# Kernel optimization log

Measured on AMD Instinct MI355X. Metric: run time of the kernel, lower is better.

Reference implementation:

```python
import jax, jax.numpy as jnp
import numpy as np

N = 100000     # total points
PBS = 500      # point_batch_size (hard-coded in module)
K = 100        # num_neighbors
KP = 15        # num_kernel_points
EPS = 1e-5


def _bn(x, g, b, axes):
    # torch BatchNorm in training mode: batch stats, biased variance
    m = jnp.mean(x, axis=axes, keepdims=True)
    v = jnp.var(x, axis=axes, keepdims=True)
    return (x - m) / jnp.sqrt(v + EPS) * g + b


def setup_inputs() -> dict:
    key = jax.random.key(0)
    ks = jax.random.split(key, 16)
    rn = lambda k, sh, s=1.0: jax.random.normal(k, sh, jnp.float32) * s
    return {
        "pts": rn(ks[0], (N, 3)),
        "normal": rn(ks[1], (N, 3)),
        "kp_points": rn(ks[2], (KP, 3)),
        "kp_weights": rn(ks[3], (KP, 3, 128), 0.3),
        "kp_sigma": jnp.float32(1.0),
        "conv1_w": rn(ks[4], (1024, 128), 128 ** -0.5),
        "conv1_b": rn(ks[5], (1024,), 0.02),
        "bn1_g": jnp.ones((1024,), jnp.float32),
        "bn1_b": jnp.zeros((1024,), jnp.float32),
        "fc1_w": rn(ks[6], (512, 1024), 1024 ** -0.5),
        "fc1_b": rn(ks[7], (512,), 0.02),
        "bn4_g": jnp.ones((512,), jnp.float32),
        "bn4_b": jnp.zeros((512,), jnp.float32),
        "fc2_w": rn(ks[8], (256, 512), 512 ** -0.5),
        "fc2_b": rn(ks[9], (256,), 0.02),
        "bn5_g": jnp.ones((256,), jnp.float32),
        "bn5_b": jnp.zeros((256,), jnp.float32),
        "fc3_w": rn(ks[10], (3, 256), 256 ** -0.5),
        "fc3_b": rn(ks[11], (3,), 0.02),
        "index": jax.random.randint(ks[12], (PBS,), 0, N, jnp.int32),
    }


def reference(pts, normal, kp_points, kp_weights, kp_sigma,
              conv1_w, conv1_b, bn1_g, bn1_b,
              fc1_w, fc1_b, bn4_g, bn4_b,
              fc2_w, fc2_b, bn5_g, bn5_b,
              fc3_w, fc3_b, index):
    sel = pts[index]                                               # [B,3]
    # L-inf pairwise distance and kNN (topk of -dist, as in the torch code)
    dist = jnp.max(jnp.abs(sel[:, None, :] - pts[None, :, :]), axis=-1)  # [B,N]
    _, nbr = jax.lax.top_k(-dist, K)                               # [B,K]
    rel = pts[nbr] - sel[:, None, :]                               # [B,K,3]

    # KPConv: gaussian weights vs kernel points, per-kernel-point linear map
    d2 = jnp.sum((rel[:, :, None, :] - kp_points[None, None]) ** 2, axis=-1)  # [B,K,KP]
    w = jnp.exp(-0.5 * d2 / (kp_sigma ** 2))
    wf = rel[:, :, None, :] * w[..., None]                         # [B,K,KP,3]
    h = jax.nn.relu(jnp.einsum('bnkc,kco->bno', wf, kp_weights))   # [B,K,128]

    # 1x1 conv 128->1024, relu then BN over (batch, points) per channel
    h = jnp.einsum('bnc,oc->bno', h, conv1_w) + conv1_b            # [B,K,1024]
    h = _bn(jax.nn.relu(h), bn1_g, bn1_b, (0, 1))
    feat = jnp.max(h, axis=1)                                      # [B,1024]

    feat = _bn(jax.nn.relu(feat @ fc1_w.T + fc1_b), bn4_g, bn4_b, (0,))
    feat = _bn(jax.nn.relu(feat @ fc2_w.T + fc2_b), bn5_g, bn5_b, (0,))
    feat = feat @ fc3_w.T + fc3_b                                  # [B,3]
    return feat, normal[index]
```

## Files before the change

kernel.cpp:

```cpp
#include <hip/hip_runtime.h>
#include <hip/hip_fp16.h>

#define NPTS 100000
#define NB 500
#define KNN 100
#define KPN 15
#define C1 128
#define C2 1024
#define C3 512
#define C4 256

typedef _Float16 half8 __attribute__((ext_vector_type(8)));
typedef float f32x4 __attribute__((ext_vector_type(4)));

__global__ __launch_bounds__(256) void gather_kernel(
    const float* __restrict__ pts, const float* __restrict__ normal,
    const int* __restrict__ index, float* __restrict__ sel,
    float* __restrict__ out2) {
  int b = blockIdx.x * 256 + threadIdx.x;
  if (b >= NB) return;
  int i = index[b];
  sel[b * 3 + 0] = pts[3 * i + 0];
  sel[b * 3 + 1] = pts[3 * i + 1];
  sel[b * 3 + 2] = pts[3 * i + 2];
  out2[b * 3 + 0] = normal[3 * i + 0];
  out2[b * 3 + 1] = normal[3 * i + 1];
  out2[b * 3 + 2] = normal[3 * i + 2];
}

#define KT 1024

__device__ __forceinline__ unsigned linf_bits(float px, float py, float pz,
                                              float sx, float sy, float sz) {
  float dx = fabsf(px - sx), dy = fabsf(py - sy), dz = fabsf(pz - sz);
  return __float_as_uint(fmaxf(fmaxf(dx, dy), dz));
}

__global__ __launch_bounds__(KT) void knn_kernel(
    const float* __restrict__ pts, const float* __restrict__ sel,
    int* __restrict__ nbr) {
  const int b = blockIdx.x;
  const int tid = threadIdx.x;
  __shared__ unsigned hist[4096];
  __shared__ unsigned chunksum[256];
  __shared__ unsigned s_prefix;
  __shared__ int s_kneed, s_base, s_cnt, s_direct, s_cnt2;
  __shared__ unsigned cand_bits[1024];
  __shared__ int cand_idx[1024];

  const float sx = sel[b * 3 + 0], sy = sel[b * 3 + 1], sz = sel[b * 3 + 2];
  const float4* base4 = (const float4*)pts;

  for (int j = tid; j < 4096; j += KT) hist[j] = 0;
  __syncthreads();
  {
    float4 c[6], n[6];
    int i0 = tid * 8;
#pragma unroll
    for (int j = 0; j < 6; ++j) c[j] = base4[(i0 * 3) / 4 + j];
    for (int it = 0; it < 12; ++it) {
      if (it + 1 < 12) {
        int i1 = (it + 1) * 8192 + tid * 8;
#pragma unroll
        for (int j = 0; j < 6; ++j) n[j] = base4[(i1 * 3) / 4 + j];
      }
      float px[8], py[8], pz[8];
      px[0] = c[0].x; py[0] = c[0].y; pz[0] = c[0].z;
      px[1] = c[0].w; py[1] = c[1].x; pz[1] = c[1].y;
      px[2] = c[1].z; py[2] = c[1].w; pz[2] = c[2].x;
      px[3] = c[2].y; py[3] = c[2].z; pz[3] = c[2].w;
      px[4] = c[3].x; py[4] = c[3].y; pz[4] = c[3].z;
      px[5] = c[3].w; py[5] = c[4].x; pz[5] = c[4].y;
      px[6] = c[4].z; py[6] = c[4].w; pz[6] = c[5].x;
      px[7] = c[5].y; py[7] = c[5].z; pz[7] = c[5].w;
#pragma unroll
      for (int j = 0; j < 8; ++j) {
        unsigned bits = linf_bits(px[j], py[j], pz[j], sx, sy, sz);
        atomicAdd(&hist[bits >> 19], 1u);
      }
#pragma unroll
      for (int j = 0; j < 6; ++j) c[j] = n[j];
    }
    for (int i = 98304 + tid; i < NPTS; i += KT) {
      unsigned bits =
          linf_bits(pts[3 * i], pts[3 * i + 1], pts[3 * i + 2], sx, sy, sz);
      atomicAdd(&hist[bits >> 19], 1u);
    }
  }

  unsigned shift = 19, prefix = 0, pendwidth = 0;
  int kneed = KNN;
  for (int pass = 0;; ++pass) {
    __syncthreads();
    if (tid < 256) {
      unsigned csum = 0;
      for (int j = 0; j < 16; ++j) csum += hist[tid * 16 + j];
      chunksum[tid] = csum;
    }
    __syncthreads();
    if (tid == 0) {
      unsigned need = (unsigned)kneed;
      unsigned cum = 0;
      int chunk = 0;
      while (chunk < 255 && cum + chunksum[chunk] < need) {
        cum += chunksum[chunk];
        ++chunk;
      }
      int bin = chunk * 16;
      while (cum + hist[bin] < need) {
        cum += hist[bin];
        ++bin;
      }
      s_kneed = (int)(need - cum);
      s_base = (int)cum;
      s_prefix = (unsigned)bin;
      s_cnt = (int)hist[bin];
    }
    __syncthreads();
    int bincnt = s_cnt;
    kneed = s_kneed;
    prefix = (pass == 0) ? s_prefix : ((prefix << pendwidth) | s_prefix);
    if (bincnt <= 1024 || shift == 0) break;
    unsigned fshift = shift;
    unsigned nshift = (shift == 19) ? 7u : 0u;
    pendwidth = (shift == 19) ? 12u : 7u;
    __syncthreads();
    for (int j = tid; j < 4096; j += KT) hist[j] = 0;
    __syncthreads();
    for (int i = tid; i < NPTS; i += KT) {
      unsigned bits =
          linf_bits(pts[3 * i], pts[3 * i + 1], pts[3 * i + 2], sx, sy, sz);
      if ((bits >> fshift) == prefix) {
        unsigned bin = (nshift == 7u) ? ((bits >> 7) & 4095u) : (bits & 127u);
        atomicAdd(&hist[bin], 1u);
      }
    }
    shift = nshift;
  }

  if (tid == 0) {
    s_direct = 0;
    s_cnt2 = 0;
  }
  __syncthreads();
  {
    float4 c[6], n[6];
    int i0 = tid * 8;
#pragma unroll
    for (int j = 0; j < 6; ++j) c[j] = base4[(i0 * 3) / 4 + j];
    for (int it = 0; it < 12; ++it) {
      if (it + 1 < 12) {
        int i1 = (it + 1) * 8192 + tid * 8;
#pragma unroll
        for (int j = 0; j < 6; ++j) n[j] = base4[(i1 * 3) / 4 + j];
      }
      float px[8], py[8], pz[8];
      px[0] = c[0].x; py[0] = c[0].y; pz[0] = c[0].z;
      px[1] = c[0].w; py[1] = c[1].x; pz[1] = c[1].y;
      px[2] = c[1].z; py[2] = c[1].w; pz[2] = c[2].x;
      px[3] = c[2].y; py[3] = c[2].z; pz[3] = c[2].w;
      px[4] = c[3].x; py[4] = c[3].y; pz[4] = c[3].z;
      px[5] = c[3].w; py[5] = c[4].x; pz[5] = c[4].y;
      px[6] = c[4].z; py[6] = c[4].w; pz[6] = c[5].x;
      px[7] = c[5].y; py[7] = c[5].z; pz[7] = c[5].w;
      int ibase = it * 8192 + tid * 8;
#pragma unroll
      for (int j = 0; j < 8; ++j) {
        unsigned bits = linf_bits(px[j], py[j], pz[j], sx, sy, sz);
        unsigned v = bits >> shift;
        if (v < prefix) {
          int pos = atomicAdd(&s_direct, 1);
          nbr[b * KNN + pos] = ibase + j;
        } else if (v == prefix) {
          int e = atomicAdd(&s_cnt2, 1);
          if (e < 1024) {
            cand_bits[e] = bits;
            cand_idx[e] = ibase + j;
          }
        }
      }
#pragma unroll
      for (int j = 0; j < 6; ++j) c[j] = n[j];
    }
    for (int i = 98304 + tid; i < NPTS; i += KT) {
      unsigned bits =
          linf_bits(pts[3 * i], pts[3 * i + 1], pts[3 * i + 2], sx, sy, sz);
      unsigned v = bits >> shift;
      if (v < prefix) {
        int pos = atomicAdd(&s_direct, 1);
        nbr[b * KNN + pos] = i;
      } else if (v == prefix) {
        int e = atomicAdd(&s_cnt2, 1);
        if (e < 1024) {
          cand_bits[e] = bits;
          cand_idx[e] = i;
        }
      }
    }
  }
  __syncthreads();

  int m = s_cnt2 < 1024 ? s_cnt2 : 1024;
  int base = s_direct;
  for (int c = tid; c < m; c += KT) {
    unsigned bc = cand_bits[c];
    int ic = cand_idx[c];
    int rank = 0;
    for (int j = 0; j < m; ++j) {
      unsigned bj = cand_bits[j];
      rank += (bj < bc || (bj == bc && cand_idx[j] < ic)) ? 1 : 0;
    }
    if (rank < kneed) nbr[b * KNN + base + rank] = ic;
  }
}

__global__ __launch_bounds__(256) void convert_kernel(
    const float* __restrict__ w1, const float* __restrict__ kpw,
    __half* __restrict__ wh, __half* __restrict__ kpwT_hi,
    __half* __restrict__ kpwT_lo) {
  int i = blockIdx.x * 256 + threadIdx.x;
  if (i < C2 * C1) wh[i] = __float2half(w1[i]);
  if (i < 128 * 64) {
    int o = i >> 6, j = i & 63;
    float v = (j < 45) ? kpw[j * 128 + o] : 0.f;
    __half hi = __float2half_rn(v);
    kpwT_hi[i] = hi;
    kpwT_lo[i] = __float2half_rn(v - __half2float(hi));
  }
}

__global__ __launch_bounds__(256) void kpconv_mfma_kernel(
    const float* __restrict__ pts, const float* __restrict__ sel,
    const int* __restrict__ nbr, const float* __restrict__ kp_points,
    const __half* __restrict__ kpwT_hi, const __half* __restrict__ kpwT_lo,
    const float* __restrict__ kp_sigma, __half* __restrict__ h) {
  const int b = blockIdx.x;
  const int tid = threadIdx.x;
  const int wave = tid >> 6, lane = tid & 63;
  const int lr = lane & 15, quad = lane >> 4;
  __shared__ __half As_hi[112 * 72];
  __shared__ __half As_lo[112 * 72];
  __shared__ __half Bs_hi[128 * 72];
  __shared__ __half Bs_lo[128 * 72];
  __shared__ float rel[100][4];
  __shared__ float kpp[48];

  for (int i = tid; i < 128 * 8; i += 256) {
    int row = i >> 3, seg = i & 7;
    *(float4*)&Bs_hi[row * 72 + seg * 8] =
        *(const float4*)&kpwT_hi[row * 64 + seg * 8];
    *(float4*)&Bs_lo[row * 72 + seg * 8] =
        *(const float4*)&kpwT_lo[row * 64 + seg * 8];
  }
  {
    float4 z = make_float4(0.f, 0.f, 0.f, 0.f);
    for (int i = tid; i < 112 * 8; i += 256) {
      int row = i >> 3, seg = i & 7;
      *(float4*)&As_hi[row * 72 + seg * 8] = z;
      *(float4*)&As_lo[row * 72 + seg * 8] = z;
    }
  }
  if (tid < 45) kpp[tid] = kp_points[tid];
  if (tid < 100) {
    int idx = nbr[b * KNN + tid];
    rel[tid][0] = pts[3 * idx + 0] - sel[b * 3 + 0];
    rel[tid][1] = pts[3 * idx + 1] - sel[b * 3 + 1];
    rel[tid][2] = pts[3 * idx + 2] - sel[b * 3 + 2];
  }
  __syncthreads();

  const float sg = kp_sigma[0];
  const float inv2s2 = -0.5f / (sg * sg);
  for (int i = tid; i < 100 * KPN; i += 256) {
    int k = i / KPN, p = i - k * KPN;
    float rx = rel[k][0] - kpp[p * 3 + 0];
    float ry = rel[k][1] - kpp[p * 3 + 1];
    float rz = rel[k][2] - kpp[p * 3 + 2];
    float w = expf(inv2s2 * (rx * rx + ry * ry + rz * rz));
#pragma unroll
    for (int c = 0; c < 3; ++c) {
      float a = rel[k][c] * w;
      __half hi = __float2half_rn(a);
      As_hi[k * 72 + p * 3 + c] = hi;
      As_lo[k * 72 + p * 3 + c] = __float2half_rn(a - __half2float(hi));
    }
  }
  __syncthreads();

  f32x4 acc[2][7];
#pragma unroll
  for (int t = 0; t < 2; ++t)
#pragma unroll
    for (int m = 0; m < 7; ++m) acc[t][m] = (f32x4)(0.f);

#pragma unroll
  for (int s = 0; s < 2; ++s) {
    half8 bhi[2], blo[2];
#pragma unroll
    for (int t = 0; t < 2; ++t) {
      int boff = ((wave * 2 + t) * 16 + lr) * 72 + s * 32 + quad * 8;
      bhi[t] = *(const half8*)&Bs_hi[boff];
      blo[t] = *(const half8*)&Bs_lo[boff];
    }
#pragma unroll
    for (int m = 0; m < 7; ++m) {
      int aoff = (m * 16 + lr) * 72 + s * 32 + quad * 8;
      half8 ahi = *(const half8*)&As_hi[aoff];
      half8 alo = *(const half8*)&As_lo[aoff];
#pragma unroll
      for (int t = 0; t < 2; ++t) {
        acc[t][m] = __builtin_amdgcn_mfma_f32_16x16x32_f16(ahi, bhi[t],
                                                           acc[t][m], 0, 0, 0);
        acc[t][m] = __builtin_amdgcn_mfma_f32_16x16x32_f16(ahi, blo[t],
                                                           acc[t][m], 0, 0, 0);
        acc[t][m] = __builtin_amdgcn_mfma_f32_16x16x32_f16(alo, bhi[t],
                                                           acc[t][m], 0, 0, 0);
      }
    }
  }

#pragma unroll
  for (int t = 0; t < 2; ++t) {
    int col = (wave * 2 + t) * 16 + lr;
#pragma unroll
    for (int m = 0; m < 7; ++m)
#pragma unroll
      for (int r = 0; r < 4; ++r) {
        int row = m * 16 + quad * 4 + r;
        if (row < 100)
          h[(b * KNN + row) * 128 + col] =
              __float2half_rn(fmaxf(acc[t][m][r], 0.f));
      }
  }
}

__global__ __launch_bounds__(256) void conv1_mfma_kernel(
    const __half* __restrict__ h16, const __half* __restrict__ wh,
    const float* __restrict__ bias, float* __restrict__ featmax,
    float* __restrict__ featmin, float* __restrict__ bnsum,
    float* __restrict__ bnsq) {
  const int b = blockIdx.y;
  const int n0 = blockIdx.x * 128;
  const int tid = threadIdx.x;
  const int wave = tid >> 6, lane = tid & 63;
  const int lr = lane & 15, quad = lane >> 4;
  __shared__ __half Hs[112 * 136];
  __shared__ __half Ws[128 * 136];

  for (int i = tid; i < 112 * 16; i += 256) {
    int row = i >> 4, seg = i & 15;
    float4 v = make_float4(0.f, 0.f, 0.f, 0.f);
    if (row < 100) v = *(const float4*)&h16[(b * 100 + row) * 128 + seg * 8];
    *(float4*)&Hs[row * 136 + seg * 8] = v;
  }
  for (int i = tid; i < 128 * 16; i += 256) {
    int row = i >> 4, seg = i & 15;
    *(float4*)&Ws[row * 136 + seg * 8] =
        *(const float4*)&wh[(n0 + row) * 128 + seg * 8];
  }
  __syncthreads();

  f32x4 acc[2][7];
#pragma unroll
  for (int t = 0; t < 2; ++t)
#pragma unroll
    for (int m = 0; m < 7; ++m) acc[t][m] = (f32x4)(0.f);

#pragma unroll
  for (int s = 0; s < 4; ++s) {
    half8 bfrag[2];
#pragma unroll
    for (int t = 0; t < 2; ++t)
      bfrag[t] =
          *(const half8*)&Ws[((wave * 2 + t) * 16 + lr) * 136 + s * 32 + quad * 8];
#pragma unroll
    for (int m = 0; m < 7; ++m) {
      half8 afrag = *(const half8*)&Hs[(m * 16 + lr) * 136 + s * 32 + quad * 8];
      acc[0][m] =
          __builtin_amdgcn_mfma_f32_16x16x32_f16(afrag, bfrag[0], acc[0][m], 0, 0, 0);
      acc[1][m] =
          __builtin_amdgcn_mfma_f32_16x16x32_f16(afrag, bfrag[1], acc[1][m], 0, 0, 0);
    }
  }

#pragma unroll
  for (int t = 0; t < 2; ++t) {
    int col = n0 + (wave * 2 + t) * 16 + lr;
    float bv = bias[col];
    float pmax = -1e30f, pmin = 1e30f, psum = 0.f, psq = 0.f;
#pragma unroll
    for (int m = 0; m < 7; ++m)
#pragma unroll
      for (int r = 0; r < 4; ++r) {
        int row = m * 16 + quad * 4 + r;
        if (row < 100) {
          float y = fmaxf(acc[t][m][r] + bv, 0.f);
          pmax = fmaxf(pmax, y);
          pmin = fminf(pmin, y);
          psum += y;
          psq += y * y;
        }
      }
    pmax = fmaxf(pmax, __shfl_xor(pmax, 16));
    pmax = fmaxf(pmax, __shfl_xor(pmax, 32));
    pmin = fminf(pmin, __shfl_xor(pmin, 16));
    pmin = fminf(pmin, __shfl_xor(pmin, 32));
    psum += __shfl_xor(psum, 16);
    psum += __shfl_xor(psum, 32);
    psq += __shfl_xor(psq, 16);
    psq += __shfl_xor(psq, 32);
    if (quad == 0) {
      featmax[b * C2 + col] = pmax;
      featmin[b * C2 + col] = pmin;
      atomicAdd(&bnsum[col], psum);
      atomicAdd(&bnsq[col], psq);
    }
  }
}

__global__ __launch_bounds__(256) void bn1max_kernel(
    const float* __restrict__ featmax, const float* __restrict__ featmin,
    const float* __restrict__ bnsum, const float* __restrict__ bnsq,
    const float* __restrict__ g, const float* __restrict__ bb,
    float* __restrict__ feat1) {
  int idx = blockIdx.x * 256 + threadIdx.x;
  if (idx >= NB * C2) return;
  int o = idx & (C2 - 1);
  const float invn = 1.f / (float)(NB * KNN);
  float m = bnsum[o] * invn;
  float v = bnsq[o] * invn - m * m;
  float a = g[o] / sqrtf(v + 1e-5f);
  float x = (a >= 0.f) ? featmax[idx] : featmin[idx];
  feat1[idx] = (x - m) * a + bb[o];
}

template <int KDIM>
__global__ __launch_bounds__(256) void fc_relu_stats_kernel(
    const float* __restrict__ x,
    const float* __restrict__ w,
    const float* __restrict__ bias, float* __restrict__ yraw,
    float* __restrict__ s, float* __restrict__ sq, int ncols) {
  const int r0 = blockIdx.x * 4;
  const int n0 = blockIdx.y * 64;
  const int tid = threadIdx.x;
  const int col = tid >> 2;
  const int row = tid & 3;
  __shared__ float xs[4][1028];
  __shared__ float ws[64][132];
  for (int f = tid; f < KDIM; f += 256) {
    int rr = f / (KDIM / 4), kq = (f % (KDIM / 4)) * 4;
    *(float4*)&xs[rr][kq] = *(const float4*)&x[(r0 + rr) * KDIM + kq];
  }
  float acc = 0.f;
  for (int kc = 0; kc < KDIM; kc += 128) {
    __syncthreads();
#pragma unroll
    for (int i = 0; i < 8; ++i) {
      int f = tid + i * 256;
      int cr = f >> 5, kq = (f & 31) * 4;
      *(float4*)&ws[cr][kq] = *(const float4*)&w[(n0 + cr) * KDIM + kc + kq];
    }
    __syncthreads();
    for (int kk = 0; kk < 128; kk += 4) {
      float4 xv = *(float4*)&xs[row][kc + kk];
      float4 wv = *(float4*)&ws[col][kk];
      acc += xv.x * wv.x + xv.y * wv.y + xv.z * wv.z + xv.w * wv.w;
    }
  }
  float y = fmaxf(acc + bias[n0 + col], 0.f);
  yraw[(r0 + row) * ncols + n0 + col] = y;
  float ys = y, y2 = y * y;
  ys += __shfl_xor(ys, 1); y2 += __shfl_xor(y2, 1);
  ys += __shfl_xor(ys, 2); y2 += __shfl_xor(y2, 2);
  if (row == 0) {
    atomicAdd(&s[n0 + col], ys);
    atomicAdd(&sq[n0 + col], y2);
  }
}

__global__ __launch_bounds__(256) void bn_finalize_kernel(
    const float* __restrict__ yraw, const float* __restrict__ s,
    const float* __restrict__ sq, const float* __restrict__ g,
    const float* __restrict__ bb, float* __restrict__ out, int ncols) {
  int idx = blockIdx.x * 256 + threadIdx.x;
  if (idx >= NB * ncols) return;
  int o = idx & (ncols - 1);
  float m = s[o] * (1.f / (float)NB);
  float v = sq[o] * (1.f / (float)NB) - m * m;
  float a = g[o] / sqrtf(v + 1e-5f);
  out[idx] = (yraw[idx] - m) * a + bb[o];
}

__global__ __launch_bounds__(256) void fc3_kernel(
    const float* __restrict__ feat, const float* __restrict__ w,
    const float* __restrict__ bias, float* __restrict__ out) {
  int idx = blockIdx.x * 256 + threadIdx.x;
  if (idx >= NB * 3) return;
  int b = idx / 3, o = idx % 3;
  float acc = 0.f;
  for (int k = 0; k < C4; ++k) acc += feat[b * C4 + k] * w[o * C4 + k];
  out[idx] = acc + bias[o];
}

extern "C" void kernel_launch(void* const* d_in, const int* in_sizes, int n_in,
                              void* d_out, int out_size, void* d_ws,
                              size_t ws_size, hipStream_t stream) {
  const float* pts = (const float*)d_in[0];
  const float* normal = (const float*)d_in[1];
  const float* kp_points = (const float*)d_in[2];
  const float* kp_weights = (const float*)d_in[3];
  const float* kp_sigma = (const float*)d_in[4];
  const float* conv1_w = (const float*)d_in[5];
  const float* conv1_b = (const float*)d_in[6];
  const float* bn1_g = (const float*)d_in[7];
  const float* bn1_b = (const float*)d_in[8];
  const float* fc1_w = (const float*)d_in[9];
  const float* fc1_b = (const float*)d_in[10];
  const float* bn4_g = (const float*)d_in[11];
  const float* bn4_b = (const float*)d_in[12];
  const float* fc2_w = (const float*)d_in[13];
  const float* fc2_b = (const float*)d_in[14];
  const float* bn5_g = (const float*)d_in[15];
  const float* bn5_b = (const float*)d_in[16];
  const float* fc3_w = (const float*)d_in[17];
  const float* fc3_b = (const float*)d_in[18];
  const int* index = (const int*)d_in[19];
  float* out = (float*)d_out;

  char* p = (char*)d_ws;
  auto carve = [&](size_t bytes) {
    void* r = (void*)p;
    p += (bytes + 255) & ~(size_t)255;
    return r;
  };
  float* sel = (float*)carve(NB * 3 * 4);
  int* nbr = (int*)carve(NB * KNN * 4);
  __half* h = (__half*)carve((size_t)NB * KNN * C1 * 2);
  __half* wh = (__half*)carve((size_t)C2 * C1 * 2);
  __half* kpwT_hi = (__half*)carve((size_t)128 * 64 * 2);
  __half* kpwT_lo = (__half*)carve((size_t)128 * 64 * 2);
  float* featmax = (float*)carve(NB * C2 * 4);
  float* featmin = (float*)carve(NB * C2 * 4);
  float* feat1 = (float*)carve(NB * C2 * 4);
  float* f2raw = (float*)carve(NB * C3 * 4);
  float* feat2 = (float*)carve(NB * C3 * 4);
  float* f3raw = (float*)carve(NB * C4 * 4);
  float* feat3 = (float*)carve(NB * C4 * 4);
  float* stats = (float*)carve((2 * C2 + 2 * C3 + 2 * C4) * 4);
  float* bnsum = stats;
  float* bnsq = stats + C2;
  float* s4 = stats + 2 * C2;
  float* sq4 = s4 + C3;
  float* s5 = sq4 + C3;
  float* sq5 = s5 + C4;

  hipMemsetAsync(stats, 0, (2 * C2 + 2 * C3 + 2 * C4) * 4, stream);

  gather_kernel<<<2, 256, 0, stream>>>(pts, normal, index, sel, out + NB * 3);
  knn_kernel<<<NB, KT, 0, stream>>>(pts, sel, nbr);
  convert_kernel<<<(C2 * C1 + 255) / 256, 256, 0, stream>>>(
      conv1_w, kp_weights, wh, kpwT_hi, kpwT_lo);
  kpconv_mfma_kernel<<<NB, 256, 0, stream>>>(pts, sel, nbr, kp_points, kpwT_hi,
                                             kpwT_lo, kp_sigma, h);
  conv1_mfma_kernel<<<dim3(8, NB), 256, 0, stream>>>(h, wh, conv1_b, featmax,
                                                     featmin, bnsum, bnsq);
  bn1max_kernel<<<(NB * C2 + 255) / 256, 256, 0, stream>>>(
      featmax, featmin, bnsum, bnsq, bn1_g, bn1_b, feat1);
  fc_relu_stats_kernel<C2><<<dim3(125, C3 / 64), 256, 0, stream>>>(
      feat1, fc1_w, fc1_b, f2raw, s4, sq4, C3);
  bn_finalize_kernel<<<(NB * C3 + 255) / 256, 256, 0, stream>>>(
      f2raw, s4, sq4, bn4_g, bn4_b, feat2, C3);
  fc_relu_stats_kernel<C3><<<dim3(125, C4 / 64), 256, 0, stream>>>(
      feat2, fc2_w, fc2_b, f3raw, s5, sq5, C4);
  bn_finalize_kernel<<<(NB * C4 + 255) / 256, 256, 0, stream>>>(
      f3raw, s5, sq5, bn5_g, bn5_b, feat3, C4);
  fc3_kernel<<<(NB * 3 + 255) / 256, 256, 0, stream>>>(feat3, fc3_w, fc3_b,
                                                       out);
}
```

Measured before the change: 287.6 us.

## Process two query points per kNN block and merge gather with weight conversion

The kNN kernel now handles two selected points per 1024-thread block, so each point-cloud load feeds two L-inf distance computations and two histograms instead of one. This halves global reads of the 100k points per query and cuts the grid to 250 blocks. Shared memory per block roughly doubles and the grid becomes smaller than before, which may reduce occupancy or leave the GPU underfilled. The gather and weight-conversion kernels are also fused into one prep kernel, saving a launch.

```diff
diff --git a/kernel.cpp b/kernel.cpp
--- a/kernel.cpp
+++ b/kernel.cpp
@@ -13,19 +13,30 @@
 typedef _Float16 half8 __attribute__((ext_vector_type(8)));
 typedef float f32x4 __attribute__((ext_vector_type(4)));
 
-__global__ __launch_bounds__(256) void gather_kernel(
+__global__ __launch_bounds__(256) void prep_kernel(
     const float* __restrict__ pts, const float* __restrict__ normal,
-    const int* __restrict__ index, float* __restrict__ sel,
-    float* __restrict__ out2) {
-  int b = blockIdx.x * 256 + threadIdx.x;
-  if (b >= NB) return;
-  int i = index[b];
-  sel[b * 3 + 0] = pts[3 * i + 0];
-  sel[b * 3 + 1] = pts[3 * i + 1];
-  sel[b * 3 + 2] = pts[3 * i + 2];
-  out2[b * 3 + 0] = normal[3 * i + 0];
-  out2[b * 3 + 1] = normal[3 * i + 1];
-  out2[b * 3 + 2] = normal[3 * i + 2];
+    const int* __restrict__ index, const float* __restrict__ w1,
+    const float* __restrict__ kpw, float* __restrict__ sel,
+    float* __restrict__ out2, __half* __restrict__ wh,
+    __half* __restrict__ kpwT_hi, __half* __restrict__ kpwT_lo) {
+  int i = blockIdx.x * 256 + threadIdx.x;
+  if (i < NB) {
+    int ix = index[i];
+    sel[i * 3 + 0] = pts[3 * ix + 0];
+    sel[i * 3 + 1] = pts[3 * ix + 1];
+    sel[i * 3 + 2] = pts[3 * ix + 2];
+    out2[i * 3 + 0] = normal[3 * ix + 0];
+    out2[i * 3 + 1] = normal[3 * ix + 1];
+    out2[i * 3 + 2] = normal[3 * ix + 2];
+  }
+  if (i < C2 * C1) wh[i] = __float2half(w1[i]);
+  if (i < 128 * 64) {
+    int o = i >> 6, j = i & 63;
+    float v = (j < 45) ? kpw[j * 128 + o] : 0.f;
+    __half hi = __float2half_rn(v);
+    kpwT_hi[i] = hi;
+    kpwT_lo[i] = __float2half_rn(v - __half2float(hi));
+  }
 }
 
 #define KT 1024
@@ -39,20 +50,25 @@
 __global__ __launch_bounds__(KT) void knn_kernel(
     const float* __restrict__ pts, const float* __restrict__ sel,
     int* __restrict__ nbr) {
-  const int b = blockIdx.x;
+  const int b0 = blockIdx.x * 2;
   const int tid = threadIdx.x;
-  __shared__ unsigned hist[4096];
-  __shared__ unsigned chunksum[256];
-  __shared__ unsigned s_prefix;
-  __shared__ int s_kneed, s_base, s_cnt, s_direct, s_cnt2;
-  __shared__ unsigned cand_bits[1024];
-  __shared__ int cand_idx[1024];
-
-  const float sx = sel[b * 3 + 0], sy = sel[b * 3 + 1], sz = sel[b * 3 + 2];
+  __shared__ unsigned hist[2][4096];
+  __shared__ unsigned chunksum[2][256];
+  __shared__ unsigned s_prefix[2];
+  __shared__ int s_kneed[2], s_cnt[2];
+  __shared__ int s_direct[2], s_cnt2[2];
+  __shared__ unsigned cand_bits[2][1024];
+  __shared__ int cand_idx[2][1024];
+
+  const float sx0 = sel[b0 * 3 + 0], sy0 = sel[b0 * 3 + 1],
+              sz0 = sel[b0 * 3 + 2];
+  const float sx1 = sel[b0 * 3 + 3], sy1 = sel[b0 * 3 + 4],
+              sz1 = sel[b0 * 3 + 5];
   const float4* base4 = (const float4*)pts;
 
-  for (int j = tid; j < 4096; j += KT) hist[j] = 0;
+  for (int j = tid; j < 2 * 4096; j += KT) ((unsigned*)hist)[j] = 0;
   __syncthreads();
+
   {
     float4 c[6], n[6];
     int i0 = tid * 8;
@@ -75,74 +91,108 @@
       px[7] = c[5].y; py[7] = c[5].z; pz[7] = c[5].w;
 #pragma unroll
       for (int j = 0; j < 8; ++j) {
-        unsigned bits = linf_bits(px[j], py[j], pz[j], sx, sy, sz);
-        atomicAdd(&hist[bits >> 19], 1u);
+        unsigned u0 = linf_bits(px[j], py[j], pz[j], sx0, sy0, sz0);
+        unsigned u1 = linf_bits(px[j], py[j], pz[j], sx1, sy1, sz1);
+        atomicAdd(&hist[0][u0 >> 19], 1u);
+        atomicAdd(&hist[1][u1 >> 19], 1u);
       }
 #pragma unroll
       for (int j = 0; j < 6; ++j) c[j] = n[j];
     }
     for (int i = 98304 + tid; i < NPTS; i += KT) {
-      unsigned bits =
-          linf_bits(pts[3 * i], pts[3 * i + 1], pts[3 * i + 2], sx, sy, sz);
-      atomicAdd(&hist[bits >> 19], 1u);
-    }
-  }
-
-  unsigned shift = 19, prefix = 0, pendwidth = 0;
-  int kneed = KNN;
+      float x = pts[3 * i], y = pts[3 * i + 1], z = pts[3 * i + 2];
+      atomicAdd(&hist[0][linf_bits(x, y, z, sx0, sy0, sz0) >> 19], 1u);
+      atomicAdd(&hist[1][linf_bits(x, y, z, sx1, sy1, sz1) >> 19], 1u);
+    }
+  }
+
+  unsigned shiftq[2] = {19u, 19u};
+  unsigned prefixq[2] = {0u, 0u};
+  unsigned pendw[2] = {0u, 0u};
+  int kneedq[2] = {KNN, KNN};
+  int activeq = 3;
   for (int pass = 0;; ++pass) {
     __syncthreads();
-    if (tid < 256) {
-      unsigned csum = 0;
-      for (int j = 0; j < 16; ++j) csum += hist[tid * 16 + j];
-      chunksum[tid] = csum;
+    if (tid < 512) {
+      int q = tid >> 8;
+      if (activeq & (1 << q)) {
+        int ch = tid & 255;
+        unsigned csum = 0;
+        for (int j = 0; j < 16; ++j) csum += hist[q][ch * 16 + j];
+        chunksum[q][ch] = csum;
+      }
     }
     __syncthreads();
-    if (tid == 0) {
-      unsigned need = (unsigned)kneed;
+    if (tid < 2 && (activeq & (1 << tid))) {
+      const int q = tid;
+      unsigned need = (unsigned)kneedq[q];
       unsigned cum = 0;
       int chunk = 0;
-      while (chunk < 255 && cum + chunksum[chunk] < need) {
-        cum += chunksum[chunk];
+      while (chunk < 255 && cum + chunksum[q][chunk] < need) {
+        cum += chunksum[q][chunk];
         ++chunk;
       }
       int bin = chunk * 16;
-      while (cum + hist[bin] < need) {
-        cum += hist[bin];
+      while (cum + hist[q][bin] < need) {
+        cum += hist[q][bin];
         ++bin;
       }
-      s_kneed = (int)(need - cum);
-      s_base = (int)cum;
-      s_prefix = (unsigned)bin;
-      s_cnt = (int)hist[bin];
+      s_kneed[q] = (int)(need - cum);
+      s_prefix[q] = (unsigned)bin;
+      s_cnt[q] = (int)hist[q][bin];
     }
     __syncthreads();
-    int bincnt = s_cnt;
-    kneed = s_kneed;
-    prefix = (pass == 0) ? s_prefix : ((prefix << pendwidth) | s_prefix);
-    if (bincnt <= 1024 || shift == 0) break;
-    unsigned fshift = shift;
-    unsigned nshift = (shift == 19) ? 7u : 0u;
-    pendwidth = (shift == 19) ? 12u : 7u;
-    __syncthreads();
-    for (int j = tid; j < 4096; j += KT) hist[j] = 0;
+    int newactive = 0;
+#pragma unroll
+    for (int q = 0; q < 2; ++q) {
+      if (!(activeq & (1 << q))) continue;
+      kneedq[q] = s_kneed[q];
+      prefixq[q] = (pass == 0) ? s_prefix[q]
+                               : ((prefixq[q] << pendw[q]) | s_prefix[q]);
+      if (s_cnt[q] > 1024 && shiftq[q] != 0u) newactive |= (1 << q);
+    }
+    if (!newactive) break;
+    for (int q = 0; q < 2; ++q)
+      if (newactive & (1 << q))
+        for (int j = tid; j < 4096; j += KT) hist[q][j] = 0;
+    unsigned fs0 = shiftq[0], fs1 = shiftq[1];
+    unsigned ns0 = (fs0 == 19u) ? 7u : 0u;
+    unsigned ns1 = (fs1 == 19u) ? 7u : 0u;
+#pragma unroll
+    for (int q = 0; q < 2; ++q)
+      if (newactive & (1 << q)) pendw[q] = (shiftq[q] == 19u) ? 12u : 7u;
     __syncthreads();
     for (int i = tid; i < NPTS; i += KT) {
-      unsigned bits =
-          linf_bits(pts[3 * i], pts[3 * i + 1], pts[3 * i + 2], sx, sy, sz);
-      if ((bits >> fshift) == prefix) {
-        unsigned bin = (nshift == 7u) ? ((bits >> 7) & 4095u) : (bits & 127u);
-        atomicAdd(&hist[bin], 1u);
-      }
-    }
-    shift = nshift;
+      float x = pts[3 * i], y = pts[3 * i + 1], z = pts[3 * i + 2];
+      if (newactive & 1) {
+        unsigned bits = linf_bits(x, y, z, sx0, sy0, sz0);
+        if ((bits >> fs0) == prefixq[0]) {
+          unsigned bin = (ns0 == 7u) ? ((bits >> 7) & 4095u) : (bits & 127u);
+          atomicAdd(&hist[0][bin], 1u);
+        }
+      }
+      if (newactive & 2) {
+        unsigned bits = linf_bits(x, y, z, sx1, sy1, sz1);
+        if ((bits >> fs1) == prefixq[1]) {
+          unsigned bin = (ns1 == 7u) ? ((bits >> 7) & 4095u) : (bits & 127u);
+          atomicAdd(&hist[1][bin], 1u);
+        }
+      }
+    }
+    if (newactive & 1) shiftq[0] = ns0;
+    if (newactive & 2) shiftq[1] = ns1;
+    activeq = newactive;
   }
 
   if (tid == 0) {
-    s_direct = 0;
-    s_cnt2 = 0;
+    s_direct[0] = 0;
+    s_direct[1] = 0;
+    s_cnt2[0] = 0;
+    s_cnt2[1] = 0;
   }
   __syncthreads();
+  const unsigned sh0 = shiftq[0], sh1 = shiftq[1];
+  const unsigned pf0 = prefixq[0], pf1 = prefixq[1];
   {
     float4 c[6], n[6];
     int i0 = tid * 8;
@@ -166,66 +216,78 @@
       int ibase = it * 8192 + tid * 8;
 #pragma unroll
       for (int j = 0; j < 8; ++j) {
-        unsigned bits = linf_bits(px[j], py[j], pz[j], sx, sy, sz);
-        unsigned v = bits >> shift;
-        if (v < prefix) {
-          int pos = atomicAdd(&s_direct, 1);
-          nbr[b * KNN + pos] = ibase + j;
-        } else if (v == prefix) {
-          int e = atomicAdd(&s_cnt2, 1);
+        unsigned u0 = linf_bits(px[j], py[j], pz[j], sx0, sy0, sz0);
+        unsigned v0 = u0 >> sh0;
+        if (v0 < pf0) {
+          int pos = atomicAdd(&s_direct[0], 1);
+          nbr[b0 * KNN + pos] = ibase + j;
+        } else if (v0 == pf0) {
+          int e = atomicAdd(&s_cnt2[0], 1);
           if (e < 1024) {
-            cand_bits[e] = bits;
-            cand_idx[e] = ibase + j;
+            cand_bits[0][e] = u0;
+            cand_idx[0][e] = ibase + j;
           }
         }
+        unsigned u1 = linf_bits(px[j], py[j], pz[j], sx1, sy1, sz1);
+        unsigned v1 = u1 >> sh1;
+        if (v1 < pf1) {
+          int pos = atomicAdd(&s_direct[1], 1);
+          nbr[(b0 + 1) * KNN + pos] = ibase + j;
+        } else if (v1 == pf1) {
+          int e = atomicAdd(&s_cnt2[1], 1);
+          if (e < 1024) {
+            cand_bits[1][e] = u1;
+            cand_idx[1][e] = ibase + j;
+          }
+        }
       }
 #pragma unroll
       for (int j = 0; j < 6; ++j) c[j] = n[j];
     }
     for (int i = 98304 + tid; i < NPTS; i += KT) {
-      unsigned bits =
-          linf_bits(pts[3 * i], pts[3 * i + 1], pts[3 * i + 2], sx, sy, sz);
-      unsigned v = bits >> shift;
-      if (v < prefix) {
-        int pos = atomicAdd(&s_direct, 1);
-        nbr[b * KNN + pos] = i;
-      } else if (v == prefix) {
-        int e = atomicAdd(&s_cnt2, 1);
+      float x = pts[3 * i], y = pts[3 * i + 1], z = pts[3 * i + 2];
+      unsigned u0 = linf_bits(x, y, z, sx0, sy0, sz0);
+      unsigned v0 = u0 >> sh0;
+      if (v0 < pf0) {
+        int pos = atomicAdd(&s_direct[0], 1);
+        nbr[b0 * KNN + pos] = i;
+      } else if (v0 == pf0) {
+        int e = atomicAdd(&s_cnt2[0], 1);
         if (e < 1024) {
-          cand_bits[e] = bits;
-          cand_idx[e] = i;
+          cand_bits[0][e] = u0;
+          cand_idx[0][e] = i;
         }
       }
+      unsigned u1 = linf_bits(x, y, z, sx1, sy1, sz1);
+      unsigned v1 = u1 >> sh1;
+      if (v1 < pf1) {
+        int pos = atomicAdd(&s_direct[1], 1);
+        nbr[(b0 + 1) * KNN + pos] = i;
+      } else if (v1 == pf1) {
+        int e = atomicAdd(&s_cnt2[1], 1);
+        if (e < 1024) {
+          cand_bits[1][e] = u1;
+          cand_idx[1][e] = i;
+        }
+      }
     }
   }
   __syncthreads();
 
-  int m = s_cnt2 < 1024 ? s_cnt2 : 1024;
-  int base = s_direct;
-  for (int c = tid; c < m; c += KT) {
-    unsigned bc = cand_bits[c];
-    int ic = cand_idx[c];
-    int rank = 0;
-    for (int j = 0; j < m; ++j) {
-      unsigned bj = cand_bits[j];
-      rank += (bj < bc || (bj == bc && cand_idx[j] < ic)) ? 1 : 0;
-    }
-    if (rank < kneed) nbr[b * KNN + base + rank] = ic;
-  }
-}
-
-__global__ __launch_bounds__(256) void convert_kernel(
-    const float* __restrict__ w1, const float* __restrict__ kpw,
-    __half* __restrict__ wh, __half* __restrict__ kpwT_hi,
-    __half* __restrict__ kpwT_lo) {
-  int i = blockIdx.x * 256 + threadIdx.x;
-  if (i < C2 * C1) wh[i] = __float2half(w1[i]);
-  if (i < 128 * 64) {
-    int o = i >> 6, j = i & 63;
-    float v = (j < 45) ? kpw[j * 128 + o] : 0.f;
-    __half hi = __float2half_rn(v);
-    kpwT_hi[i] = hi;
-    kpwT_lo[i] = __float2half_rn(v - __half2float(hi));
+#pragma unroll
+  for (int q = 0; q < 2; ++q) {
+    int m = s_cnt2[q] < 1024 ? s_cnt2[q] : 1024;
+    int base = s_direct[q];
+    for (int c2 = tid; c2 < m; c2 += KT) {
+      unsigned bc = cand_bits[q][c2];
+      int ic = cand_idx[q][c2];
+      int rank = 0;
+      for (int j = 0; j < m; ++j) {
+        unsigned bj = cand_bits[q][j];
+        rank += (bj < bc || (bj == bc && cand_idx[q][j] < ic)) ? 1 : 0;
+      }
+      if (rank < kneedq[q]) nbr[(b0 + q) * KNN + base + rank] = ic;
+    }
   }
 }
 
@@ -556,10 +618,10 @@
 
   hipMemsetAsync(stats, 0, (2 * C2 + 2 * C3 + 2 * C4) * 4, stream);
 
-  gather_kernel<<<2, 256, 0, stream>>>(pts, normal, index, sel, out + NB * 3);
-  knn_kernel<<<NB, KT, 0, stream>>>(pts, sel, nbr);
-  convert_kernel<<<(C2 * C1 + 255) / 256, 256, 0, stream>>>(
-      conv1_w, kp_weights, wh, kpwT_hi, kpwT_lo);
+  prep_kernel<<<(C2 * C1 + 255) / 256, 256, 0, stream>>>(
+      pts, normal, index, conv1_w, kp_weights, sel, out + NB * 3, wh, kpwT_hi,
+      kpwT_lo);
+  knn_kernel<<<NB / 2, KT, 0, stream>>>(pts, sel, nbr);
   kpconv_mfma_kernel<<<NB, 256, 0, stream>>>(pts, sel, nbr, kp_points, kpwT_hi,
                                              kpwT_lo, kp_sigma, h);
   conv1_mfma_kernel<<<dim3(8, NB), 256, 0, stream>>>(h, wh, conv1_b, featmax,
```

Result: no change. 282.4 us (-1.8%).

## Replace brute-force radix-select kNN with uniform grid spatial index search

Applied to the files above, without the earlier changes.

Builds a 64^3 uniform grid over points (histogram, three-stage scan, scatter into cell-sorted float4 array), then each query expands a cube of cells until at least K points are found. It takes a distance bound from a histogram of those candidates and rescans the cells within that bound before ranking. This avoids scanning all 100k points per query several times. It relies on a fixed grid extent of ±5 (points outside are clamped into edge cells) and on a candidate cap of 2048, which could truncate in dense regions. The gather and weight conversion kernels are also merged into one prep kernel. The grid buffers reuse the h buffer's memory before kpconv writes it.

```diff
diff --git a/kernel.cpp b/kernel.cpp
--- a/kernel.cpp
+++ b/kernel.cpp
@@ -10,215 +10,31 @@
 #define C3 512
 #define C4 256
 
+#define G 64
+#define NCELLS (G * G * G)
+#define GB 5.0f
+#define GINVH ((float)G / (2.f * GB))
+#define CAND_CAP 2048
+
 typedef _Float16 half8 __attribute__((ext_vector_type(8)));
 typedef float f32x4 __attribute__((ext_vector_type(4)));
 
-__global__ __launch_bounds__(256) void gather_kernel(
+__global__ __launch_bounds__(256) void prep_kernel(
     const float* __restrict__ pts, const float* __restrict__ normal,
-    const int* __restrict__ index, float* __restrict__ sel,
-    float* __restrict__ out2) {
-  int b = blockIdx.x * 256 + threadIdx.x;
-  if (b >= NB) return;
-  int i = index[b];
-  sel[b * 3 + 0] = pts[3 * i + 0];
-  sel[b * 3 + 1] = pts[3 * i + 1];
-  sel[b * 3 + 2] = pts[3 * i + 2];
-  out2[b * 3 + 0] = normal[3 * i + 0];
-  out2[b * 3 + 1] = normal[3 * i + 1];
-  out2[b * 3 + 2] = normal[3 * i + 2];
-}
-
-#define KT 1024
-
-__device__ __forceinline__ unsigned linf_bits(float px, float py, float pz,
-                                              float sx, float sy, float sz) {
-  float dx = fabsf(px - sx), dy = fabsf(py - sy), dz = fabsf(pz - sz);
-  return __float_as_uint(fmaxf(fmaxf(dx, dy), dz));
-}
-
-__global__ __launch_bounds__(KT) void knn_kernel(
-    const float* __restrict__ pts, const float* __restrict__ sel,
-    int* __restrict__ nbr) {
-  const int b = blockIdx.x;
-  const int tid = threadIdx.x;
-  __shared__ unsigned hist[4096];
-  __shared__ unsigned chunksum[256];
-  __shared__ unsigned s_prefix;
-  __shared__ int s_kneed, s_base, s_cnt, s_direct, s_cnt2;
-  __shared__ unsigned cand_bits[1024];
-  __shared__ int cand_idx[1024];
-
-  const float sx = sel[b * 3 + 0], sy = sel[b * 3 + 1], sz = sel[b * 3 + 2];
-  const float4* base4 = (const float4*)pts;
-
-  for (int j = tid; j < 4096; j += KT) hist[j] = 0;
-  __syncthreads();
-  {
-    float4 c[6], n[6];
-    int i0 = tid * 8;
-#pragma unroll
-    for (int j = 0; j < 6; ++j) c[j] = base4[(i0 * 3) / 4 + j];
-    for (int it = 0; it < 12; ++it) {
-      if (it + 1 < 12) {
-        int i1 = (it + 1) * 8192 + tid * 8;
-#pragma unroll
-        for (int j = 0; j < 6; ++j) n[j] = base4[(i1 * 3) / 4 + j];
-      }
-      float px[8], py[8], pz[8];
-      px[0] = c[0].x; py[0] = c[0].y; pz[0] = c[0].z;
-      px[1] = c[0].w; py[1] = c[1].x; pz[1] = c[1].y;
-      px[2] = c[1].z; py[2] = c[1].w; pz[2] = c[2].x;
-      px[3] = c[2].y; py[3] = c[2].z; pz[3] = c[2].w;
-      px[4] = c[3].x; py[4] = c[3].y; pz[4] = c[3].z;
-      px[5] = c[3].w; py[5] = c[4].x; pz[5] = c[4].y;
-      px[6] = c[4].z; py[6] = c[4].w; pz[6] = c[5].x;
-      px[7] = c[5].y; py[7] = c[5].z; pz[7] = c[5].w;
-#pragma unroll
-      for (int j = 0; j < 8; ++j) {
-        unsigned bits = linf_bits(px[j], py[j], pz[j], sx, sy, sz);
-        atomicAdd(&hist[bits >> 19], 1u);
-      }
-#pragma unroll
-      for (int j = 0; j < 6; ++j) c[j] = n[j];
-    }
-    for (int i = 98304 + tid; i < NPTS; i += KT) {
-      unsigned bits =
-          linf_bits(pts[3 * i], pts[3 * i + 1], pts[3 * i + 2], sx, sy, sz);
-      atomicAdd(&hist[bits >> 19], 1u);
-    }
-  }
-
-  unsigned shift = 19, prefix = 0, pendwidth = 0;
-  int kneed = KNN;
-  for (int pass = 0;; ++pass) {
-    __syncthreads();
-    if (tid < 256) {
-      unsigned csum = 0;
-      for (int j = 0; j < 16; ++j) csum += hist[tid * 16 + j];
-      chunksum[tid] = csum;
-    }
-    __syncthreads();
-    if (tid == 0) {
-      unsigned need = (unsigned)kneed;
-      unsigned cum = 0;
-      int chunk = 0;
-      while (chunk < 255 && cum + chunksum[chunk] < need) {
-        cum += chunksum[chunk];
-        ++chunk;
-      }
-      int bin = chunk * 16;
-      while (cum + hist[bin] < need) {
-        cum += hist[bin];
-        ++bin;
-      }
-      s_kneed = (int)(need - cum);
-      s_base = (int)cum;
-      s_prefix = (unsigned)bin;
-      s_cnt = (int)hist[bin];
-    }
-    __syncthreads();
-    int bincnt = s_cnt;
-    kneed = s_kneed;
-    prefix = (pass == 0) ? s_prefix : ((prefix << pendwidth) | s_prefix);
-    if (bincnt <= 1024 || shift == 0) break;
-    unsigned fshift = shift;
-    unsigned nshift = (shift == 19) ? 7u : 0u;
-    pendwidth = (shift == 19) ? 12u : 7u;
-    __syncthreads();
-    for (int j = tid; j < 4096; j += KT) hist[j] = 0;
-    __syncthreads();
-    for (int i = tid; i < NPTS; i += KT) {
-      unsigned bits =
-          linf_bits(pts[3 * i], pts[3 * i + 1], pts[3 * i + 2], sx, sy, sz);
-      if ((bits >> fshift) == prefix) {
-        unsigned bin = (nshift == 7u) ? ((bits >> 7) & 4095u) : (bits & 127u);
-        atomicAdd(&hist[bin], 1u);
-      }
-    }
-    shift = nshift;
-  }
-
-  if (tid == 0) {
-    s_direct = 0;
-    s_cnt2 = 0;
-  }
-  __syncthreads();
-  {
-    float4 c[6], n[6];
-    int i0 = tid * 8;
-#pragma unroll
-    for (int j = 0; j < 6; ++j) c[j] = base4[(i0 * 3) / 4 + j];
-    for (int it = 0; it < 12; ++it) {
-      if (it + 1 < 12) {
-        int i1 = (it + 1) * 8192 + tid * 8;
-#pragma unroll
-        for (int j = 0; j < 6; ++j) n[j] = base4[(i1 * 3) / 4 + j];
-      }
-      float px[8], py[8], pz[8];
-      px[0] = c[0].x; py[0] = c[0].y; pz[0] = c[0].z;
-      px[1] = c[0].w; py[1] = c[1].x; pz[1] = c[1].y;
-      px[2] = c[1].z; py[2] = c[1].w; pz[2] = c[2].x;
-      px[3] = c[2].y; py[3] = c[2].z; pz[3] = c[2].w;
-      px[4] = c[3].x; py[4] = c[3].y; pz[4] = c[3].z;
-      px[5] = c[3].w; py[5] = c[4].x; pz[5] = c[4].y;
-      px[6] = c[4].z; py[6] = c[4].w; pz[6] = c[5].x;
-      px[7] = c[5].y; py[7] = c[5].z; pz[7] = c[5].w;
-      int ibase = it * 8192 + tid * 8;
-#pragma unroll
-      for (int j = 0; j < 8; ++j) {
-        unsigned bits = linf_bits(px[j], py[j], pz[j], sx, sy, sz);
-        unsigned v = bits >> shift;
-        if (v < prefix) {
-          int pos = atomicAdd(&s_direct, 1);
-          nbr[b * KNN + pos] = ibase + j;
-        } else if (v == prefix) {
-          int e = atomicAdd(&s_cnt2, 1);
-          if (e < 1024) {
-            cand_bits[e] = bits;
-            cand_idx[e] = ibase + j;
-          }
-        }
-      }
-#pragma unroll
-      for (int j = 0; j < 6; ++j) c[j] = n[j];
-    }
-    for (int i = 98304 + tid; i < NPTS; i += KT) {
-      unsigned bits =
-          linf_bits(pts[3 * i], pts[3 * i + 1], pts[3 * i + 2], sx, sy, sz);
-      unsigned v = bits >> shift;
-      if (v < prefix) {
-        int pos = atomicAdd(&s_direct, 1);
-        nbr[b * KNN + pos] = i;
-      } else if (v == prefix) {
-        int e = atomicAdd(&s_cnt2, 1);
-        if (e < 1024) {
-          cand_bits[e] = bits;
-          cand_idx[e] = i;
-        }
-      }
-    }
-  }
-  __syncthreads();
-
-  int m = s_cnt2 < 1024 ? s_cnt2 : 1024;
-  int base = s_direct;
-  for (int c = tid; c < m; c += KT) {
-    unsigned bc = cand_bits[c];
-    int ic = cand_idx[c];
-    int rank = 0;
-    for (int j = 0; j < m; ++j) {
-      unsigned bj = cand_bits[j];
-      rank += (bj < bc || (bj == bc && cand_idx[j] < ic)) ? 1 : 0;
-    }
-    if (rank < kneed) nbr[b * KNN + base + rank] = ic;
-  }
-}
-
-__global__ __launch_bounds__(256) void convert_kernel(
-    const float* __restrict__ w1, const float* __restrict__ kpw,
-    __half* __restrict__ wh, __half* __restrict__ kpwT_hi,
-    __half* __restrict__ kpwT_lo) {
+    const int* __restrict__ index, const float* __restrict__ w1,
+    const float* __restrict__ kpw, float* __restrict__ sel,
+    float* __restrict__ out2, __half* __restrict__ wh,
+    __half* __restrict__ kpwT_hi, __half* __restrict__ kpwT_lo) {
   int i = blockIdx.x * 256 + threadIdx.x;
+  if (i < NB) {
+    int ix = index[i];
+    sel[i * 3 + 0] = pts[3 * ix + 0];
+    sel[i * 3 + 1] = pts[3 * ix + 1];
+    sel[i * 3 + 2] = pts[3 * ix + 2];
+    out2[i * 3 + 0] = normal[3 * ix + 0];
+    out2[i * 3 + 1] = normal[3 * ix + 1];
+    out2[i * 3 + 2] = normal[3 * ix + 2];
+  }
   if (i < C2 * C1) wh[i] = __float2half(w1[i]);
   if (i < 128 * 64) {
     int o = i >> 6, j = i & 63;
@@ -226,6 +42,244 @@
     __half hi = __float2half_rn(v);
     kpwT_hi[i] = hi;
     kpwT_lo[i] = __float2half_rn(v - __half2float(hi));
+  }
+}
+
+__device__ __forceinline__ int cell_coord(float x) {
+  int c = (int)floorf((x + GB) * GINVH);
+  return min(max(c, 0), G - 1);
+}
+__device__ __forceinline__ int cell_of(float x, float y, float z) {
+  return (cell_coord(x) << 12) | (cell_coord(y) << 6) | cell_coord(z);
+}
+
+__global__ __launch_bounds__(256) void grid_hist_kernel(
+    const float* __restrict__ pts, unsigned* __restrict__ cnt) {
+  int i = blockIdx.x * 256 + threadIdx.x;
+  if (i >= NPTS) return;
+  atomicAdd(&cnt[cell_of(pts[3 * i], pts[3 * i + 1], pts[3 * i + 2])], 1u);
+}
+
+__global__ __launch_bounds__(256) void grid_scan1_kernel(
+    const unsigned* __restrict__ cnt, unsigned* __restrict__ cursor,
+    unsigned* __restrict__ chunktot) {
+  const int tid = threadIdx.x;
+  int base = blockIdx.x * 1024 + tid * 4;
+  unsigned c0 = cnt[base], c1 = cnt[base + 1], c2 = cnt[base + 2],
+           c3 = cnt[base + 3];
+  unsigned tot = c0 + c1 + c2 + c3;
+  __shared__ unsigned sb[256];
+  sb[tid] = tot;
+  __syncthreads();
+  for (int off = 1; off < 256; off <<= 1) {
+    unsigned add = (tid >= off) ? sb[tid - off] : 0u;
+    __syncthreads();
+    sb[tid] += add;
+    __syncthreads();
+  }
+  unsigned excl = sb[tid] - tot;
+  cursor[base] = excl;
+  cursor[base + 1] = excl + c0;
+  cursor[base + 2] = excl + c0 + c1;
+  cursor[base + 3] = excl + c0 + c1 + c2;
+  if (tid == 255) chunktot[blockIdx.x] = sb[255];
+}
+
+__global__ __launch_bounds__(256) void grid_scan2_kernel(
+    const unsigned* __restrict__ chunktot, unsigned* __restrict__ chunkoff) {
+  const int tid = threadIdx.x;
+  unsigned v = chunktot[tid];
+  __shared__ unsigned sb[256];
+  sb[tid] = v;
+  __syncthreads();
+  for (int off = 1; off < 256; off <<= 1) {
+    unsigned add = (tid >= off) ? sb[tid - off] : 0u;
+    __syncthreads();
+    sb[tid] += add;
+    __syncthreads();
+  }
+  chunkoff[tid] = sb[tid] - v;
+}
+
+__global__ __launch_bounds__(256) void grid_scan3_kernel(
+    unsigned* __restrict__ cursor, const unsigned* __restrict__ chunkoff) {
+  unsigned off = chunkoff[blockIdx.x];
+  int base = blockIdx.x * 1024 + threadIdx.x * 4;
+#pragma unroll
+  for (int j = 0; j < 4; ++j) cursor[base + j] += off;
+}
+
+__global__ __launch_bounds__(256) void grid_scatter_kernel(
+    const float* __restrict__ pts, unsigned* __restrict__ cursor,
+    float4* __restrict__ sorted) {
+  int i = blockIdx.x * 256 + threadIdx.x;
+  if (i >= NPTS) return;
+  float x = pts[3 * i], y = pts[3 * i + 1], z = pts[3 * i + 2];
+  unsigned pos = atomicAdd(&cursor[cell_of(x, y, z)], 1u);
+  sorted[pos] = make_float4(x, y, z, __int_as_float(i));
+}
+
+__device__ __forceinline__ unsigned linf_bits(float px, float py, float pz,
+                                              float sx, float sy, float sz) {
+  float dx = fabsf(px - sx), dy = fabsf(py - sy), dz = fabsf(pz - sz);
+  return __float_as_uint(fmaxf(fmaxf(dx, dy), dz));
+}
+
+__global__ __launch_bounds__(256) void knn_kernel(
+    const float4* __restrict__ sorted, const unsigned* __restrict__ cnt,
+    const unsigned* __restrict__ cursor,
+    const float* __restrict__ sel, int* __restrict__ nbr) {
+  const int b = blockIdx.x;
+  const int tid = threadIdx.x;
+  __shared__ unsigned cbits[CAND_CAP];
+  __shared__ int cidx[CAND_CAP];
+  __shared__ unsigned hist[4096];
+  __shared__ unsigned scanbuf[256];
+  __shared__ int s_total, s_m, s_mc, s_chunk;
+  __shared__ unsigned s_excl, s_bub;
+
+  const float qx = sel[b * 3 + 0], qy = sel[b * 3 + 1], qz = sel[b * 3 + 2];
+  const int qcx = cell_coord(qx), qcy = cell_coord(qy), qcz = cell_coord(qz);
+
+  int s = 0;
+  int xlo, xhi, ylo, yhi, zlo, zhi;
+  for (;;) {
+    if (tid == 0) s_total = 0;
+    __syncthreads();
+    xlo = max(qcx - s, 0); xhi = min(qcx + s, G - 1);
+    ylo = max(qcy - s, 0); yhi = min(qcy + s, G - 1);
+    zlo = max(qcz - s, 0); zhi = min(qcz + s, G - 1);
+    int nx = xhi - xlo + 1, ny = yhi - ylo + 1, nz = zhi - zlo + 1;
+    int ncell = nx * ny * nz;
+    unsigned local = 0;
+    for (int ci = tid; ci < ncell; ci += 256) {
+      int cz = ci % nz;
+      int r = ci / nz;
+      int cy = r % ny;
+      int cx = r / ny;
+      local += cnt[((xlo + cx) << 12) | ((ylo + cy) << 6) | (zlo + cz)];
+    }
+#pragma unroll
+    for (int off = 32; off; off >>= 1) local += __shfl_down(local, off);
+    if ((tid & 63) == 0) atomicAdd(&s_total, (int)local);
+    __syncthreads();
+    if (s_total >= KNN || (xlo == 0 && ylo == 0 && zlo == 0 && xhi == G - 1 &&
+                           yhi == G - 1 && zhi == G - 1))
+      break;
+    ++s;
+    __syncthreads();
+  }
+
+  if (tid == 0) s_m = 0;
+  __syncthreads();
+  {
+    int nx = xhi - xlo + 1, ny = yhi - ylo + 1, nz = zhi - zlo + 1;
+    int ncell = nx * ny * nz;
+    for (int ci = tid; ci < ncell; ci += 256) {
+      int cz = ci % nz;
+      int r = ci / nz;
+      int cy = r % ny;
+      int cx = r / ny;
+      int cell = ((xlo + cx) << 12) | ((ylo + cy) << 6) | (zlo + cz);
+      unsigned end = cursor[cell];
+      unsigned beg = end - cnt[cell];
+      for (unsigned p = beg; p < end; ++p) {
+        float4 f = sorted[p];
+        unsigned bits = linf_bits(f.x, f.y, f.z, qx, qy, qz);
+        int e = atomicAdd(&s_m, 1);
+        if (e < CAND_CAP) {
+          cbits[e] = bits;
+          cidx[e] = __float_as_int(f.w);
+        }
+      }
+    }
+  }
+  __syncthreads();
+  int m = s_m < CAND_CAP ? s_m : CAND_CAP;
+
+  for (int j = tid; j < 4096; j += 256) hist[j] = 0;
+  __syncthreads();
+  for (int e = tid; e < m; e += 256) atomicAdd(&hist[cbits[e] >> 19], 1u);
+  __syncthreads();
+  unsigned csum = 0;
+  {
+    int c0 = tid * 16;
+#pragma unroll
+    for (int j = 0; j < 16; ++j) csum += hist[c0 + j];
+  }
+  scanbuf[tid] = csum;
+  __syncthreads();
+  for (int off = 1; off < 256; off <<= 1) {
+    unsigned add = (tid >= off) ? scanbuf[tid - off] : 0u;
+    __syncthreads();
+    scanbuf[tid] += add;
+    __syncthreads();
+  }
+  {
+    unsigned incl = scanbuf[tid], excl = incl - csum;
+    if (excl < KNN && KNN <= incl) {
+      s_chunk = tid;
+      s_excl = excl;
+    }
+  }
+  __syncthreads();
+  if (tid == 0) {
+    unsigned cum = s_excl;
+    int bin = s_chunk * 16;
+    while (cum + hist[bin] < KNN) {
+      cum += hist[bin];
+      ++bin;
+    }
+    s_bub = (unsigned)(bin + 1) << 19;
+  }
+  __syncthreads();
+
+  const unsigned bub = s_bub;
+  const float dub = __uint_as_float(bub);
+  if (tid == 0) s_mc = 0;
+  __syncthreads();
+  {
+    int xlo2 = min(max((int)floorf((qx - dub + GB) * GINVH), 0), G - 1);
+    int xhi2 = min(max((int)floorf((qx + dub + GB) * GINVH), 0), G - 1);
+    int ylo2 = min(max((int)floorf((qy - dub + GB) * GINVH), 0), G - 1);
+    int yhi2 = min(max((int)floorf((qy + dub + GB) * GINVH), 0), G - 1);
+    int zlo2 = min(max((int)floorf((qz - dub + GB) * GINVH), 0), G - 1);
+    int zhi2 = min(max((int)floorf((qz + dub + GB) * GINVH), 0), G - 1);
+    int nx = xhi2 - xlo2 + 1, ny = yhi2 - ylo2 + 1, nz = zhi2 - zlo2 + 1;
+    int ncell = nx * ny * nz;
+    for (int ci = tid; ci < ncell; ci += 256) {
+      int cz = ci % nz;
+      int r = ci / nz;
+      int cy = r % ny;
+      int cx = r / ny;
+      int cell = ((xlo2 + cx) << 12) | ((ylo2 + cy) << 6) | (zlo2 + cz);
+      unsigned end = cursor[cell];
+      unsigned beg = end - cnt[cell];
+      for (unsigned p = beg; p < end; ++p) {
+        float4 f = sorted[p];
+        unsigned bits = linf_bits(f.x, f.y, f.z, qx, qy, qz);
+        if (bits < bub) {
+          int e = atomicAdd(&s_mc, 1);
+          if (e < CAND_CAP) {
+            cbits[e] = bits;
+            cidx[e] = __float_as_int(f.w);
+          }
+        }
+      }
+    }
+  }
+  __syncthreads();
+  int mc = s_mc < CAND_CAP ? s_mc : CAND_CAP;
+
+  for (int c = tid; c < mc; c += 256) {
+    unsigned bc = cbits[c];
+    int ic = cidx[c];
+    int rank = 0;
+    for (int j = 0; j < mc; ++j) {
+      unsigned bj = cbits[j];
+      rank += (bj < bc || (bj == bc && cidx[j] < ic)) ? 1 : 0;
+    }
+    if (rank < KNN) nbr[b * KNN + rank] = ic;
   }
 }
 
@@ -554,12 +608,34 @@
   float* s5 = sq4 + C3;
   float* sq5 = s5 + C4;
 
-  hipMemsetAsync(stats, 0, (2 * C2 + 2 * C3 + 2 * C4) * 4, stream);
-
-  gather_kernel<<<2, 256, 0, stream>>>(pts, normal, index, sel, out + NB * 3);
-  knn_kernel<<<NB, KT, 0, stream>>>(pts, sel, nbr);
-  convert_kernel<<<(C2 * C1 + 255) / 256, 256, 0, stream>>>(
-      conv1_w, kp_weights, wh, kpwT_hi, kpwT_lo);
+  {
+    char* gp = (char*)h;
+    auto gcarve = [&](size_t bytes) {
+      void* r = (void*)gp;
+      gp += (bytes + 255) & ~(size_t)255;
+      return r;
+    };
+    unsigned* cellcnt = (unsigned*)gcarve((size_t)NCELLS * 4);
+    unsigned* cellcur = (unsigned*)gcarve((size_t)NCELLS * 4);
+    unsigned* chunktot = (unsigned*)gcarve(256 * 4);
+    unsigned* chunkoff = (unsigned*)gcarve(256 * 4);
+    float4* sortedpts = (float4*)gcarve((size_t)NPTS * 16);
+
+    hipMemsetAsync(stats, 0, (2 * C2 + 2 * C3 + 2 * C4) * 4, stream);
+    hipMemsetAsync(cellcnt, 0, (size_t)NCELLS * 4, stream);
+
+    prep_kernel<<<(C2 * C1 + 255) / 256, 256, 0, stream>>>(
+        pts, normal, index, conv1_w, kp_weights, sel, out + NB * 3, wh,
+        kpwT_hi, kpwT_lo);
+    grid_hist_kernel<<<(NPTS + 255) / 256, 256, 0, stream>>>(pts, cellcnt);
+    grid_scan1_kernel<<<256, 256, 0, stream>>>(cellcnt, cellcur, chunktot);
+    grid_scan2_kernel<<<1, 256, 0, stream>>>(chunktot, chunkoff);
+    grid_scan3_kernel<<<256, 256, 0, stream>>>(cellcur, chunkoff);
+    grid_scatter_kernel<<<(NPTS + 255) / 256, 256, 0, stream>>>(pts, cellcur,
+                                                                sortedpts);
+    knn_kernel<<<NB, 256, 0, stream>>>(sortedpts, cellcnt, cellcur, sel, nbr);
+  }
+
   kpconv_mfma_kernel<<<NB, 256, 0, stream>>>(pts, sel, nbr, kp_points, kpwT_hi,
                                              kpwT_lo, kp_sigma, h);
   conv1_mfma_kernel<<<dim3(8, NB), 256, 0, stream>>>(h, wh, conv1_b, featmax,
```

Result: slower. 298.1 us (+3.6%).
